# Performance work log

Measured on AMD Instinct MI355X. Metric: run time of the kernel, lower is better.

## Reference

```python
import jax, jax.numpy as jnp
import numpy as np

K = 5
BN_EPS = 1e-5


def _knn(xyz1, xyz2, embedding_lens):
    # squared pairwise distances [B, N, S]
    d2 = (jnp.sum(xyz1 ** 2, -1)[:, :, None]
          + jnp.sum(xyz2 ** 2, -1)[:, None, :]
          - 2.0 * jnp.einsum('bnc,bsc->bns', xyz1, xyz2))
    S = xyz2.shape[1]
    valid2 = jnp.arange(S)[None, :] < embedding_lens[:, None]  # [B, S]
    d2 = jnp.where(valid2[:, None, :], d2, jnp.float32(1e10))
    neg, idx = jax.lax.top_k(-d2, K)  # K smallest distances
    return -neg, idx  # squared dists [B,N,K], indices [B,N,K]


def _masked_bn(x, mask_f, gamma, beta):
    # x: [B, N, C]; mask_f: [B, N, 1] float; stats over valid positions only
    cnt = jnp.sum(mask_f)
    mean = jnp.sum(x * mask_f, axis=(0, 1)) / cnt
    var = jnp.sum(((x - mean) ** 2) * mask_f, axis=(0, 1)) / cnt
    return (x - mean) * jax.lax.rsqrt(var + BN_EPS) * gamma + beta


def setup_inputs() -> dict:
    key = jax.random.key(0)
    ks = jax.random.split(key, 8)
    B, N, S, D1, D2 = 16, 2048, 512, 384, 384
    xyz1 = jax.random.normal(ks[0], (B, N, 3), jnp.float32)
    xyz2 = jax.random.normal(ks[1], (B, S, 3), jnp.float32)
    points1 = jax.random.normal(ks[2], (B, N, D1), jnp.float32)
    points2 = jax.random.normal(ks[3], (B, S, D2), jnp.float32)
    point_lens = jax.random.randint(ks[4], (B,), N // 2, N + 1).astype(jnp.int32)
    embedding_lens = jax.random.randint(ks[5], (B,), S // 2, S + 1).astype(jnp.int32)
    point_mask = jnp.arange(N)[None, :] < point_lens[:, None]  # [B, N] bool
    Cin = D1 + D2
    W0 = jax.random.normal(ks[6], (768, Cin), jnp.float32) * (1.0 / np.sqrt(Cin))
    W1 = jax.random.normal(ks[7], (384, 768), jnp.float32) * (1.0 / np.sqrt(768))
    return dict(xyz1=xyz1, xyz2=xyz2, points1=points1, points2=points2,
                point_lens=point_lens, embedding_lens=embedding_lens,
                point_mask=point_mask,
                W0=W0, g0=jnp.ones((768,), jnp.float32), b0=jnp.zeros((768,), jnp.float32),
                W1=W1, g1=jnp.ones((384,), jnp.float32), b1=jnp.zeros((384,), jnp.float32))


def reference(xyz1, xyz2, points1, points2, point_lens, embedding_lens,
              point_mask, W0, g0, b0, W1, g1, b1):
    B, N, _ = xyz1.shape
    D2 = points2.shape[-1]
    dists, idx = _knn(xyz1[..., :3], xyz2, embedding_lens)
    eps = jnp.finfo(dists.dtype).eps
    dist_recip = 1.0 / (dists + eps)                    # [B, N, K]
    weight = dist_recip / jnp.sum(dist_recip, axis=2, keepdims=True)
    # masked gather: points2[b, idx[b,n,k], :] -> [B, N, K, D2]
    gathered = jnp.take_along_axis(points2, idx.reshape(B, N * K)[..., None],
                                   axis=1).reshape(B, N, K, D2)
    interp = jnp.sum(gathered * weight[..., None], axis=2)  # [B, N, D2]
    x = jnp.concatenate([points1, interp], axis=-1)          # [B, N, D1+D2]
    mask_f = point_mask.astype(x.dtype)[..., None]           # [B, N, 1]
    for W, g, b in ((W0, g0, b0), (W1, g1, b1)):
        x = jnp.einsum('bnc,dc->bnd', x, W)  # 1x1 conv, no bias
        x = jax.nn.relu(_masked_bn(x, mask_f, g, b))
    return x
```

## Files before the change

### kernel.cpp

```cpp
#include <hip/hip_runtime.h>
#include <cstdint>
#include <cstddef>

typedef unsigned short u16;
typedef __bf16 bf16x8 __attribute__((ext_vector_type(8)));
typedef float    f32x4 __attribute__((ext_vector_type(4)));
typedef unsigned int u32x4 __attribute__((ext_vector_type(4)));

constexpr int BB   = 16;
constexpr int NN   = 2048;
constexpr int SS   = 512;
constexpr int DD   = 384;
constexpr int CIN  = 768;
constexpr int HID  = 768;
constexpr int OUTC = 384;
constexpr int MROWS = BB * NN;
constexpr float KNN_EPS = 1.1920929e-07f;
constexpr float BN_EPS  = 1e-5f;

constexpr size_t OFF_W0B  = 0;
constexpr size_t OFF_W1B  = OFF_W0B  + (size_t)HID*CIN*2;
constexpr size_t OFF_IDX  = OFF_W1B  + (size_t)OUTC*HID*2;
constexpr size_t OFF_WGT  = OFF_IDX  + (size_t)MROWS*5*4;
constexpr size_t OFF_SUM1 = OFF_WGT  + (size_t)MROWS*5*4;
constexpr size_t OFF_SUM2 = OFF_SUM1 + (size_t)HID*2*4;
constexpr size_t OFF_COEF1= OFF_SUM2 + (size_t)OUTC*2*4;
constexpr size_t OFF_COEF2= OFF_COEF1+ (size_t)HID*2*4;
constexpr size_t OFF_XCAT = OFF_COEF2+ (size_t)OUTC*2*4;
constexpr size_t OFF_H1   = OFF_XCAT + (size_t)MROWS*CIN*2;

__device__ inline float bf2f(u16 u){ unsigned int i = ((unsigned int)u)<<16; float f; __builtin_memcpy(&f,&i,4); return f; }
__device__ inline u16 f2bf(float f){ unsigned int x; __builtin_memcpy(&x,&f,4);
  unsigned int r = (x + 0x7fffu + ((x>>16)&1u)) >> 16; return (u16)r; }

__device__ inline void async16(const void* g, void* l){
  __builtin_amdgcn_global_load_lds((const __attribute__((address_space(1))) void*)g,
                                   (__attribute__((address_space(3))) void*)l, 16, 0, 0);
}

__global__ void cvtw_kernel(const float* __restrict__ W0, const float* __restrict__ W1,
                            u16* __restrict__ W0b, u16* __restrict__ W1b){
  int t = blockIdx.x*256 + threadIdx.x;
  if (t < HID*CIN)  W0b[t] = f2bf(W0[t]);
  if (t < OUTC*HID) W1b[t] = f2bf(W1[t]);
}

__global__ __launch_bounds__(256) void knn_kernel(const float* __restrict__ xyz1,
                                                  const float* __restrict__ xyz2,
                                                  const int* __restrict__ elens,
                                                  int* __restrict__ idxO, float* __restrict__ wO){
  __shared__ f32x4 sp[SS];
  const int tid = threadIdx.x;
  const int wv = tid >> 6, lane = tid & 63;
  const int wg = blockIdx.x*4 + wv;
  const int b = wg >> 11;
  const int n = wg & (NN-1);
  for (int s = tid; s < SS; s += 256){
    float x = xyz2[((size_t)b*SS + s)*3 + 0];
    float y = xyz2[((size_t)b*SS + s)*3 + 1];
    float z = xyz2[((size_t)b*SS + s)*3 + 2];
    f32x4 v; v[0]=x; v[1]=y; v[2]=z; v[3]=x*x+y*y+z*z;
    sp[s]=v;
  }
  __syncthreads();
  const size_t qoff = ((size_t)b*NN + n)*3;
  const float qx = xyz1[qoff+0], qy = xyz1[qoff+1], qz = xyz1[qoff+2];
  const float qq = qx*qx + qy*qy + qz*qz;
  const int Sl = elens[b];

  float d0=1e30f,d1=1e30f,d2v=1e30f,d3=1e30f,d4=1e30f;
  int   i0=0,i1=0,i2=0,i3=0,i4=0;
  #pragma unroll
  for (int j=0;j<8;j++){
    const int s = lane + j*64;
    f32x4 v = sp[s];
    float d = (s < Sl) ? (qq + v[3] - 2.f*(qx*v[0] + qy*v[1] + qz*v[2])) : 1e30f;
    bool lt4=d<d4, lt3=d<d3, lt2=d<d2v, lt1=d<d1, lt0=d<d0;
    float nd4 = lt3 ? d3 : (lt4 ? d : d4); int ni4 = lt3 ? i3 : (lt4 ? s : i4);
    float nd3 = lt2 ? d2v: (lt3 ? d : d3); int ni3 = lt2 ? i2 : (lt3 ? s : i3);
    float nd2 = lt1 ? d1 : (lt2 ? d : d2v);int ni2 = lt1 ? i1 : (lt2 ? s : i2);
    float nd1 = lt0 ? d0 : (lt1 ? d : d1); int ni1 = lt0 ? i0 : (lt1 ? s : i1);
    float nd0 = lt0 ? d  : d0;             int ni0 = lt0 ? s  : i0;
    d4=nd4;i4=ni4; d3=nd3;i3=ni3; d2v=nd2;i2=ni2; d1=nd1;i1=ni1; d0=nd0;i0=ni0;
  }
  float outd[5]; int outi[5];
  #pragma unroll
  for (int r=0;r<5;r++){
    float bd = d0; int bs = i0;
    #pragma unroll
    for (int m=1;m<64;m<<=1){
      float od = __shfl_xor(bd, m, 64);
      int   os = __shfl_xor(bs, m, 64);
      if (od < bd || (od == bd && os < bs)){ bd = od; bs = os; }
    }
    outd[r]=bd; outi[r]=bs;
    if (d0 == bd && i0 == bs){ d0=d1;i0=i1; d1=d2v;i1=i2; d2v=d3;i2=i3; d3=d4;i3=i4; d4=1e30f;i4=0; }
  }
  if (lane == 0){
    float r0=1.f/(outd[0]+KNN_EPS), r1=1.f/(outd[1]+KNN_EPS), r2=1.f/(outd[2]+KNN_EPS),
          r3=1.f/(outd[3]+KNN_EPS), r4=1.f/(outd[4]+KNN_EPS);
    float inv = 1.f/(r0+r1+r2+r3+r4);
    size_t base = (size_t)wg*5;
    idxO[base+0]=outi[0]; idxO[base+1]=outi[1]; idxO[base+2]=outi[2]; idxO[base+3]=outi[3]; idxO[base+4]=outi[4];
    wO[base+0]=r0*inv; wO[base+1]=r1*inv; wO[base+2]=r2*inv; wO[base+3]=r3*inv; wO[base+4]=r4*inv;
  }
}

__global__ __launch_bounds__(384) void xcat_kernel(const float* __restrict__ p1,
                                                   const float* __restrict__ p2,
                                                   const int* __restrict__ idx,
                                                   const float* __restrict__ wgt,
                                                   u16* __restrict__ xcat){
  const int c = threadIdx.x;
  const int rowbase = blockIdx.x*8;
  for (int i=0;i<8;i++){
    const int row = rowbase + i;
    const int b = row >> 11;
    float v1 = p1[(size_t)row*DD + c];
    xcat[(size_t)row*CIN + c] = f2bf(v1);
    float acc = 0.f;
    size_t ib = (size_t)row*5;
    #pragma unroll
    for (int k=0;k<5;k++){
      int id = idx[ib+k]; float w = wgt[ib+k];
      acc += w * p2[((size_t)b*SS + id)*DD + c];
    }
    xcat[(size_t)row*CIN + DD + c] = f2bf(acc);
  }
}

__global__ __launch_bounds__(512) void gemm1_kernel(const u16* __restrict__ A,
                                                    const u16* __restrict__ Bw,
                                                    u16* __restrict__ Cout,
                                                    const int* __restrict__ plen,
                                                    float* __restrict__ sums){
  constexpr int K   = CIN;
  constexpr int NC  = HID;
  constexpr int GXX = NC/128;
  constexpr int NT  = K/32;
  constexpr int NWG = (MROWS/256)*GXX;
  constexpr int CPX = NWG/8;
  __shared__ u16 Ash[3][8192];
  __shared__ u16 Bsh[2][4096];

  const int tid  = threadIdx.x;
  const int lane = tid & 63, wv = tid >> 6;
  const int wr = wv >> 2, wc = wv & 3;
  const int l15 = lane & 15, l16 = lane >> 4;
  const int swz = (l15 >> 1) & 3;

  const int logical = (blockIdx.x & 7)*CPX + (blockIdx.x >> 3);
  const int bn = logical % GXX, bm = logical / GXX;

  const int chA0 = tid,      rA0 = chA0 >> 2, kA0 = (chA0 & 3) ^ ((chA0 >> 3) & 3);
  const int chA1 = 512+tid,  rA1 = chA1 >> 2, kA1 = (chA1 & 3) ^ ((chA1 >> 3) & 3);
  const int chB  = tid,      rB  = chB  >> 2, kB  = (chB  & 3) ^ ((chB  >> 3) & 3);
  const u16* gA0 = A  + (size_t)(bm*256 + rA0)*K + kA0*8;
  const u16* gA1 = A  + (size_t)(bm*256 + rA1)*K + kA1*8;
  const u16* gB  = Bw + (size_t)(bn*128 + rB )*K + kB*8;

  auto stageA = [&](int tt, int ab){
    async16(gA0 + tt*32, (char*)&Ash[ab][0] + wv*1024);
    async16(gA1 + tt*32, (char*)&Ash[ab][0] + 8192 + wv*1024);
  };
  auto stageB = [&](int tt, int bb){
    async16(gB + tt*32, (char*)&Bsh[bb][0] + wv*1024);
  };

  int aoff[8], boff[2];
  #pragma unroll
  for (int m=0;m<8;m++) aoff[m] = (wr*128 + m*16 + l15)*32 + ((l16 ^ swz) << 3);
  #pragma unroll
  for (int n=0;n<2;n++) boff[n] = (wc*32 + n*16 + l15)*32 + ((l16 ^ swz) << 3);

  f32x4 acc[8][2] = {};

  stageA(0, 0); stageB(0, 0); stageA(1, 1);
  asm volatile("s_waitcnt vmcnt(2)" ::: "memory");
  __builtin_amdgcn_s_barrier();

  auto step = [&](int t, int ab, int bb, int bbn, int abn2){
    if (t+1 < NT) stageB(t+1, bbn);
    if (t+2 < NT) stageA(t+2, abn2);
    bf16x8 af[8], bfr[2];
    #pragma unroll
    for (int n=0;n<2;n++) bfr[n] = *reinterpret_cast<const bf16x8*>(&Bsh[bb][boff[n]]);
    #pragma unroll
    for (int m=0;m<8;m++) af[m] = *reinterpret_cast<const bf16x8*>(&Ash[ab][aoff[m]]);
    __builtin_amdgcn_s_setprio(1);
    #pragma unroll
    for (int m=0;m<8;m++)
      #pragma unroll
      for (int n=0;n<2;n++)
        acc[m][n] = __builtin_amdgcn_mfma_f32_16x16x32_bf16(af[m], bfr[n], acc[m][n], 0, 0, 0);
    __builtin_amdgcn_s_setprio(0);
    asm volatile("s_waitcnt vmcnt(2)" ::: "memory");
    __builtin_amdgcn_s_barrier();
  };

  for (int t0=0; t0<NT; t0+=6){
    step(t0+0, 0, 0, 1, 2);
    step(t0+1, 1, 1, 0, 0);
    step(t0+2, 2, 0, 1, 1);
    step(t0+3, 0, 1, 0, 2);
    step(t0+4, 1, 0, 1, 0);
    step(t0+5, 2, 1, 0, 1);
  }

  #pragma unroll
  for (int m=0;m<8;m++){
    int r0 = bm*256 + wr*128 + m*16 + l16*4;
    #pragma unroll
    for (int n=0;n<2;n++){
      int c = bn*128 + wc*32 + n*16 + l15;
      #pragma unroll
      for (int r=0;r<4;r++)
        Cout[(size_t)(r0+r)*NC + c] = f2bf(acc[m][n][r]);
    }
  }

  const int pl = plen[bm >> 3];
  const int rbase = (bm & 7)*256 + wr*128 + l16*4;
  float cs[2] = {0.f,0.f}, cs2[2] = {0.f,0.f};
  #pragma unroll
  for (int m=0;m<8;m++){
    #pragma unroll
    for (int r=0;r<4;r++){
      if (rbase + m*16 + r < pl){
        #pragma unroll
        for (int n=0;n<2;n++){
          float v = acc[m][n][r];
          cs[n] += v; cs2[n] += v*v;
        }
      }
    }
  }
  #pragma unroll
  for (int n=0;n<2;n++){
    cs[n]  += __shfl_xor(cs[n], 16, 64);  cs[n]  += __shfl_xor(cs[n], 32, 64);
    cs2[n] += __shfl_xor(cs2[n], 16, 64); cs2[n] += __shfl_xor(cs2[n], 32, 64);
  }
  float* lsum = (float*)&Ash[0][0];
  if (tid < 256) lsum[tid] = 0.f;
  __syncthreads();
  if (l16 == 0){
    #pragma unroll
    for (int n=0;n<2;n++){
      int col = wc*32 + n*16 + l15;
      atomicAdd(&lsum[col], cs[n]);
      atomicAdd(&lsum[128 + col], cs2[n]);
    }
  }
  __syncthreads();
  if (tid < 128)       atomicAdd(&sums[bn*128 + tid], lsum[tid]);
  else if (tid < 256)  atomicAdd(&sums[NC + bn*128 + (tid-128)], lsum[tid]);
}

__global__ __launch_bounds__(256) void gemm2_kernel(const u16* __restrict__ A,
                                                    const u16* __restrict__ Bw,
                                                    float* __restrict__ Cout,
                                                    const int* __restrict__ plen,
                                                    float* __restrict__ sums,
                                                    const float* __restrict__ cf){
  constexpr int GX = 3;
  constexpr int K  = HID;
  constexpr int NC = GX*128;
  constexpr int NSTEP = K/32;
  constexpr int NWG = GX*256;
  constexpr int CPX = NWG/8;
  __shared__ u16 As[2][128*32];
  __shared__ u16 Bs[2][128*32];
  const int tid  = threadIdx.x;
  const int lane = tid & 63, wv = tid >> 6;
  const int wr = wv >> 1, wc = wv & 1;
  const int l15 = lane & 15, l16 = lane >> 4;

  const int logical = (blockIdx.x & 7)*CPX + (blockIdx.x >> 3);
  const int bn = logical % GX, bm = logical / GX;

  int rowS[2], c8S[2];
  const u16* Ab[2]; const u16* Bb[2];
  #pragma unroll
  for (int j=0;j<2;j++){
    int ch = j*256 + wv*64 + lane;
    rowS[j] = ch >> 2; c8S[j] = ch & 3;
    Ab[j] = A  + (size_t)(bm*128 + rowS[j])*K + c8S[j]*8;
    Bb[j] = Bw + (size_t)(bn*128 + rowS[j])*K + c8S[j]*8;
  }

  auto stageB = [&](int nb, int kt){
    #pragma unroll
    for (int j=0;j<2;j++)
      async16(Bb[j] + kt*32, (char*)&Bs[nb][0] + (j*256 + wv*64)*16);
  };
  u32x4 hv[2];
  auto loadA = [&](int kt){
    #pragma unroll
    for (int j=0;j<2;j++)
      hv[j] = *reinterpret_cast<const u32x4*>(Ab[j] + kt*32);
  };
  auto bnwrite = [&](int nb, int kt){
    #pragma unroll
    for (int j=0;j<2;j++){
      const int k0 = kt*32 + c8S[j]*8;
      float av[8], bv[8];
      *reinterpret_cast<f32x4*>(av)   = *reinterpret_cast<const f32x4*>(cf + k0);
      *reinterpret_cast<f32x4*>(av+4) = *reinterpret_cast<const f32x4*>(cf + k0 + 4);
      *reinterpret_cast<f32x4*>(bv)   = *reinterpret_cast<const f32x4*>(cf + K + k0);
      *reinterpret_cast<f32x4*>(bv+4) = *reinterpret_cast<const f32x4*>(cf + K + k0 + 4);
      u32x4 v = hv[j]; u32x4 o;
      #pragma unroll
      for (int q=0;q<4;q++){
        float lo = bf2f((u16)(v[q] & 0xffffu));
        float hi = bf2f((u16)(v[q] >> 16));
        lo = fmaxf(lo*av[2*q]   + bv[2*q],   0.f);
        hi = fmaxf(hi*av[2*q+1] + bv[2*q+1], 0.f);
        o[q] = (unsigned int)f2bf(lo) | ((unsigned int)f2bf(hi) << 16);
      }
      *reinterpret_cast<u32x4*>((char*)&As[nb][0] + (j*256 + wv*64)*16 + lane*16) = o;
    }
  };

  f32x4 acc[4][4] = {};

  loadA(0);
  stageB(0, 0);
  bnwrite(0, 0);
  __syncthreads();

  int cur = 0;
  for (int kt=0; kt<NSTEP; ++kt){
    const bool pf = (kt+1 < NSTEP);
    if (pf){
      loadA(kt+1);
      stageB(cur^1, kt+1);
    }
    bf16x8 af[4], bfr[4];
    #pragma unroll
    for (int m=0;m<4;m++){
      int r = wr*64 + m*16 + l15;
      af[m] = *reinterpret_cast<const bf16x8*>(&As[cur][r*32 + l16*8]);
    }
    #pragma unroll
    for (int n=0;n<4;n++){
      int c = wc*64 + n*16 + l15;
      bfr[n] = *reinterpret_cast<const bf16x8*>(&Bs[cur][c*32 + l16*8]);
    }
    #pragma unroll
    for (int m=0;m<4;m++)
      #pragma unroll
      for (int n=0;n<4;n++)
        acc[m][n] = __builtin_amdgcn_mfma_f32_16x16x32_bf16(af[m], bfr[n], acc[m][n], 0, 0, 0);
    if (pf) bnwrite(cur^1, kt+1);
    __syncthreads();
    cur ^= 1;
  }

  #pragma unroll
  for (int m=0;m<4;m++){
    int r0 = bm*128 + wr*64 + m*16 + l16*4;
    #pragma unroll
    for (int n=0;n<4;n++){
      int c = bn*128 + wc*64 + n*16 + l15;
      #pragma unroll
      for (int r=0;r<4;r++)
        Cout[(size_t)(r0+r)*NC + c] = acc[m][n][r];
    }
  }

  const int pl = plen[bm >> 4];
  const int rbase = (bm & 15)*128 + wr*64 + l16*4;
  float cs[4] = {0.f,0.f,0.f,0.f}, cs2[4] = {0.f,0.f,0.f,0.f};
  #pragma unroll
  for (int m=0;m<4;m++){
    #pragma unroll
    for (int r=0;r<4;r++){
      if (rbase + m*16 + r < pl){
        #pragma unroll
        for (int n=0;n<4;n++){
          float v = acc[m][n][r];
          cs[n] += v; cs2[n] += v*v;
        }
      }
    }
  }
  #pragma unroll
  for (int n=0;n<4;n++){
    cs[n]  += __shfl_xor(cs[n], 16, 64);  cs[n]  += __shfl_xor(cs[n], 32, 64);
    cs2[n] += __shfl_xor(cs2[n], 16, 64); cs2[n] += __shfl_xor(cs2[n], 32, 64);
  }
  float* lsum = (float*)&As[0][0];
  lsum[tid] = 0.f;
  __syncthreads();
  if (l16 == 0){
    #pragma unroll
    for (int n=0;n<4;n++){
      int col = wc*64 + n*16 + l15;
      atomicAdd(&lsum[col], cs[n]);
      atomicAdd(&lsum[128 + col], cs2[n]);
    }
  }
  __syncthreads();
  if (tid < 128)       atomicAdd(&sums[bn*128 + tid], lsum[tid]);
  else                 atomicAdd(&sums[NC + bn*128 + (tid-128)], lsum[tid]);
}

__global__ void coef_kernel(const float* __restrict__ sums, const int* __restrict__ plen,
                            const float* __restrict__ g, const float* __restrict__ bta,
                            float* __restrict__ coef, int C){
  int c = threadIdx.x;
  if (c >= C) return;
  float cnt = 0.f;
  for (int b=0;b<BB;b++) cnt += (float)plen[b];
  float mean = sums[c] / cnt;
  float var  = sums[C + c] / cnt - mean*mean;
  var = fmaxf(var, 0.f);
  float a = g[c] * rsqrtf(var + BN_EPS);
  coef[c] = a;
  coef[C + c] = bta[c] - mean*a;
}

__global__ __launch_bounds__(256) void final_kernel(float* __restrict__ Y,
                                                    const float* __restrict__ coef){
  size_t t = (size_t)blockIdx.x*256 + threadIdx.x;
  size_t f = t*4;
  int c = (int)(f % (size_t)OUTC);
  f32x4 v = *reinterpret_cast<const f32x4*>(Y + f);
  #pragma unroll
  for (int j=0;j<4;j++)
    v[j] = fmaxf(v[j]*coef[c+j] + coef[OUTC+c+j], 0.f);
  *reinterpret_cast<f32x4*>(Y + f) = v;
}

extern "C" void kernel_launch(void* const* d_in, const int* in_sizes, int n_in,
                              void* d_out, int out_size, void* d_ws, size_t ws_size,
                              hipStream_t stream){
  (void)in_sizes; (void)n_in; (void)out_size; (void)ws_size;
  const float* xyz1 = (const float*)d_in[0];
  const float* xyz2 = (const float*)d_in[1];
  const float* p1   = (const float*)d_in[2];
  const float* p2   = (const float*)d_in[3];
  const int*   plen = (const int*)d_in[4];
  const int*   elen = (const int*)d_in[5];
  const float* W0   = (const float*)d_in[7];
  const float* g0   = (const float*)d_in[8];
  const float* b0   = (const float*)d_in[9];
  const float* W1   = (const float*)d_in[10];
  const float* g1   = (const float*)d_in[11];
  const float* b1   = (const float*)d_in[12];
  float* out = (float*)d_out;
  char*  ws  = (char*)d_ws;

  u16*   W0b  = (u16*)  (ws + OFF_W0B);
  u16*   W1b  = (u16*)  (ws + OFF_W1B);
  int*   idxb = (int*)  (ws + OFF_IDX);
  float* wgtb = (float*)(ws + OFF_WGT);
  float* sum1 = (float*)(ws + OFF_SUM1);
  float* sum2 = (float*)(ws + OFF_SUM2);
  float* coef1= (float*)(ws + OFF_COEF1);
  float* coef2= (float*)(ws + OFF_COEF2);
  u16*   xcat = (u16*)  (ws + OFF_XCAT);
  u16*   h1   = (u16*)  (ws + OFF_H1);

  hipMemsetAsync(ws + OFF_SUM1, 0, (size_t)(HID*2 + OUTC*2)*4, stream);

  cvtw_kernel<<<(HID*CIN + 255)/256, 256, 0, stream>>>(W0, W1, W0b, W1b);
  knn_kernel<<<MROWS/4, 256, 0, stream>>>(xyz1, xyz2, elen, idxb, wgtb);
  xcat_kernel<<<MROWS/8, 384, 0, stream>>>(p1, p2, idxb, wgtb, xcat);

  gemm1_kernel<<<(MROWS/256)*(HID/128), 512, 0, stream>>>(xcat, W0b, h1, plen, sum1);
  coef_kernel<<<1, HID, 0, stream>>>(sum1, plen, g0, b0, coef1, HID);

  gemm2_kernel<<<3*256, 256, 0, stream>>>(h1, W1b, out, plen, sum2, coef1);
  coef_kernel<<<1, OUTC, 0, stream>>>(sum2, plen, g1, b1, coef2, OUTC);
  final_kernel<<<(size_t)MROWS*OUTC/4/256, 256, 0, stream>>>(out, coef2);
}
```

Before: 209.0 us.

## Retile gemm1 to 128x128 tiles and fuse final BN/ReLU into cooperative gemm2

gemm1 moves from 256x128 tiles with 512 threads and a triple-buffered A to 128x128 tiles with 256 threads, double buffering and a split-phase MFMA schedule, which raises workgroup count and occupancy. gemm2 becomes a cooperative kernel that keeps its accumulators in registers, does a grid-wide sync after the column-statistics atomics, then computes the BN coefficients and writes ReLU'd output directly. This removes the separate coef and final kernels and the fp32 output round trip. The cost is a grid barrier that needs all 768 blocks resident, with a fallback to the old three-kernel path if the cooperative launch fails.

```diff
diff --git a/kernel.cpp b/kernel.cpp
--- a/kernel.cpp
+++ b/kernel.cpp
@@ -1,6 +1,9 @@
 #include <hip/hip_runtime.h>
+#include <hip/hip_cooperative_groups.h>
 #include <cstdint>
 #include <cstddef>
+
+namespace cg = cooperative_groups;
 
 typedef unsigned short u16;
 typedef __bf16 bf16x8 __attribute__((ext_vector_type(8)));
@@ -129,106 +132,125 @@
   }
 }
 
-__global__ __launch_bounds__(512) void gemm1_kernel(const u16* __restrict__ A,
-                                                    const u16* __restrict__ Bw,
-                                                    u16* __restrict__ Cout,
-                                                    const int* __restrict__ plen,
-                                                    float* __restrict__ sums){
+__global__ __launch_bounds__(256, 4) void gemm1_kernel(const u16* __restrict__ A,
+                                                       const u16* __restrict__ Bw,
+                                                       u16* __restrict__ Cout,
+                                                       const int* __restrict__ plen,
+                                                       float* __restrict__ sums){
   constexpr int K   = CIN;
   constexpr int NC  = HID;
-  constexpr int GXX = NC/128;
+  constexpr int GX  = NC/128;
   constexpr int NT  = K/32;
-  constexpr int NWG = (MROWS/256)*GXX;
+  constexpr int NWG = GX*256;
   constexpr int CPX = NWG/8;
-  __shared__ u16 Ash[3][8192];
-  __shared__ u16 Bsh[2][4096];
-
+  __shared__ u16 Ash[2][128*32];
+  __shared__ u16 Bsh[2][128*32];
   const int tid  = threadIdx.x;
   const int lane = tid & 63, wv = tid >> 6;
-  const int wr = wv >> 2, wc = wv & 3;
+  const int wr = wv >> 1, wc = wv & 1;
   const int l15 = lane & 15, l16 = lane >> 4;
   const int swz = (l15 >> 1) & 3;
 
   const int logical = (blockIdx.x & 7)*CPX + (blockIdx.x >> 3);
-  const int bn = logical % GXX, bm = logical / GXX;
-
-  const int chA0 = tid,      rA0 = chA0 >> 2, kA0 = (chA0 & 3) ^ ((chA0 >> 3) & 3);
-  const int chA1 = 512+tid,  rA1 = chA1 >> 2, kA1 = (chA1 & 3) ^ ((chA1 >> 3) & 3);
-  const int chB  = tid,      rB  = chB  >> 2, kB  = (chB  & 3) ^ ((chB  >> 3) & 3);
-  const u16* gA0 = A  + (size_t)(bm*256 + rA0)*K + kA0*8;
-  const u16* gA1 = A  + (size_t)(bm*256 + rA1)*K + kA1*8;
-  const u16* gB  = Bw + (size_t)(bn*128 + rB )*K + kB*8;
-
-  auto stageA = [&](int tt, int ab){
-    async16(gA0 + tt*32, (char*)&Ash[ab][0] + wv*1024);
-    async16(gA1 + tt*32, (char*)&Ash[ab][0] + 8192 + wv*1024);
+  const int bn = logical % GX, bm = logical / GX;
+
+  const int srow = tid >> 2;
+  const int sk4  = (tid & 3) ^ ((tid >> 3) & 3);
+  const u16* gA = A  + (size_t)(bm*128 + srow)*K + sk4*8;
+  const u16* gB = Bw + (size_t)(bn*128 + srow)*K + sk4*8;
+  const int dst0 = (wv*64)*16;
+  const int dst1 = (256 + wv*64)*16;
+
+  auto stageA = [&](int tt, int bi){
+    async16(gA + tt*32,        (char*)&Ash[bi][0] + dst0);
+    async16(gA + tt*32 + 64*K, (char*)&Ash[bi][0] + dst1);
   };
-  auto stageB = [&](int tt, int bb){
-    async16(gB + tt*32, (char*)&Bsh[bb][0] + wv*1024);
+  auto stageB = [&](int tt, int bi){
+    async16(gB + tt*32,        (char*)&Bsh[bi][0] + dst0);
+    async16(gB + tt*32 + 64*K, (char*)&Bsh[bi][0] + dst1);
   };
 
-  int aoff[8], boff[2];
-  #pragma unroll
-  for (int m=0;m<8;m++) aoff[m] = (wr*128 + m*16 + l15)*32 + ((l16 ^ swz) << 3);
-  #pragma unroll
-  for (int n=0;n<2;n++) boff[n] = (wc*32 + n*16 + l15)*32 + ((l16 ^ swz) << 3);
-
-  f32x4 acc[8][2] = {};
-
-  stageA(0, 0); stageB(0, 0); stageA(1, 1);
-  asm volatile("s_waitcnt vmcnt(2)" ::: "memory");
+  int aoff[4], boff[4];
+  #pragma unroll
+  for (int m=0;m<4;m++) aoff[m] = (wr*64 + m*16 + l15)*32 + ((l16 ^ swz) << 3);
+  #pragma unroll
+  for (int n=0;n<4;n++) boff[n] = (wc*64 + n*16 + l15)*32 + ((l16 ^ swz) << 3);
+
+  f32x4 acc[4][4] = {};
+
+  stageA(0,0); stageB(0,0); stageA(1,1); stageB(1,1);
+  asm volatile("s_waitcnt vmcnt(4)" ::: "memory");
   __builtin_amdgcn_s_barrier();
-
-  auto step = [&](int t, int ab, int bb, int bbn, int abn2){
-    if (t+1 < NT) stageB(t+1, bbn);
-    if (t+2 < NT) stageA(t+2, abn2);
-    bf16x8 af[8], bfr[2];
-    #pragma unroll
-    for (int n=0;n<2;n++) bfr[n] = *reinterpret_cast<const bf16x8*>(&Bsh[bb][boff[n]]);
-    #pragma unroll
-    for (int m=0;m<8;m++) af[m] = *reinterpret_cast<const bf16x8*>(&Ash[ab][aoff[m]]);
+  __builtin_amdgcn_sched_barrier(0);
+
+  for (int t=0; t<NT; ++t){
+    const int cur = t & 1;
+    const int tt = (t+2 < NT) ? (t+2) : (NT-1);
+    bf16x8 af0 = *reinterpret_cast<const bf16x8*>(&Ash[cur][aoff[0]]);
+    bf16x8 af1 = *reinterpret_cast<const bf16x8*>(&Ash[cur][aoff[1]]);
+    bf16x8 af2 = *reinterpret_cast<const bf16x8*>(&Ash[cur][aoff[2]]);
+    bf16x8 af3 = *reinterpret_cast<const bf16x8*>(&Ash[cur][aoff[3]]);
+    bf16x8 bv0 = *reinterpret_cast<const bf16x8*>(&Bsh[cur][boff[0]]);
+    bf16x8 bv1 = *reinterpret_cast<const bf16x8*>(&Bsh[cur][boff[1]]);
+    asm volatile("s_waitcnt lgkmcnt(0)" ::: "memory");
+    __builtin_amdgcn_s_barrier();
+    __builtin_amdgcn_sched_barrier(0);
+    stageA(tt, cur);
     __builtin_amdgcn_s_setprio(1);
-    #pragma unroll
-    for (int m=0;m<8;m++)
-      #pragma unroll
-      for (int n=0;n<2;n++)
-        acc[m][n] = __builtin_amdgcn_mfma_f32_16x16x32_bf16(af[m], bfr[n], acc[m][n], 0, 0, 0);
+    acc[0][0] = __builtin_amdgcn_mfma_f32_16x16x32_bf16(af0, bv0, acc[0][0], 0,0,0);
+    acc[1][0] = __builtin_amdgcn_mfma_f32_16x16x32_bf16(af1, bv0, acc[1][0], 0,0,0);
+    acc[2][0] = __builtin_amdgcn_mfma_f32_16x16x32_bf16(af2, bv0, acc[2][0], 0,0,0);
+    acc[3][0] = __builtin_amdgcn_mfma_f32_16x16x32_bf16(af3, bv0, acc[3][0], 0,0,0);
+    acc[0][1] = __builtin_amdgcn_mfma_f32_16x16x32_bf16(af0, bv1, acc[0][1], 0,0,0);
+    acc[1][1] = __builtin_amdgcn_mfma_f32_16x16x32_bf16(af1, bv1, acc[1][1], 0,0,0);
+    acc[2][1] = __builtin_amdgcn_mfma_f32_16x16x32_bf16(af2, bv1, acc[2][1], 0,0,0);
+    acc[3][1] = __builtin_amdgcn_mfma_f32_16x16x32_bf16(af3, bv1, acc[3][1], 0,0,0);
     __builtin_amdgcn_s_setprio(0);
-    asm volatile("s_waitcnt vmcnt(2)" ::: "memory");
+    bf16x8 bv2 = *reinterpret_cast<const bf16x8*>(&Bsh[cur][boff[2]]);
+    bf16x8 bv3 = *reinterpret_cast<const bf16x8*>(&Bsh[cur][boff[3]]);
+    asm volatile("s_waitcnt lgkmcnt(0)" ::: "memory");
     __builtin_amdgcn_s_barrier();
-  };
-
-  for (int t0=0; t0<NT; t0+=6){
-    step(t0+0, 0, 0, 1, 2);
-    step(t0+1, 1, 1, 0, 0);
-    step(t0+2, 2, 0, 1, 1);
-    step(t0+3, 0, 1, 0, 2);
-    step(t0+4, 1, 0, 1, 0);
-    step(t0+5, 2, 1, 0, 1);
-  }
-
-  #pragma unroll
-  for (int m=0;m<8;m++){
-    int r0 = bm*256 + wr*128 + m*16 + l16*4;
-    #pragma unroll
-    for (int n=0;n<2;n++){
-      int c = bn*128 + wc*32 + n*16 + l15;
+    __builtin_amdgcn_sched_barrier(0);
+    stageB(tt, cur);
+    __builtin_amdgcn_s_setprio(1);
+    acc[0][2] = __builtin_amdgcn_mfma_f32_16x16x32_bf16(af0, bv2, acc[0][2], 0,0,0);
+    acc[1][2] = __builtin_amdgcn_mfma_f32_16x16x32_bf16(af1, bv2, acc[1][2], 0,0,0);
+    acc[2][2] = __builtin_amdgcn_mfma_f32_16x16x32_bf16(af2, bv2, acc[2][2], 0,0,0);
+    acc[3][2] = __builtin_amdgcn_mfma_f32_16x16x32_bf16(af3, bv2, acc[3][2], 0,0,0);
+    acc[0][3] = __builtin_amdgcn_mfma_f32_16x16x32_bf16(af0, bv3, acc[0][3], 0,0,0);
+    acc[1][3] = __builtin_amdgcn_mfma_f32_16x16x32_bf16(af1, bv3, acc[1][3], 0,0,0);
+    acc[2][3] = __builtin_amdgcn_mfma_f32_16x16x32_bf16(af2, bv3, acc[2][3], 0,0,0);
+    acc[3][3] = __builtin_amdgcn_mfma_f32_16x16x32_bf16(af3, bv3, acc[3][3], 0,0,0);
+    __builtin_amdgcn_s_setprio(0);
+    asm volatile("s_waitcnt vmcnt(4)" ::: "memory");
+    __builtin_amdgcn_s_barrier();
+    __builtin_amdgcn_sched_barrier(0);
+  }
+  asm volatile("s_waitcnt vmcnt(0)" ::: "memory");
+  __syncthreads();
+
+  #pragma unroll
+  for (int m=0;m<4;m++){
+    int r0 = bm*128 + wr*64 + m*16 + l16*4;
+    #pragma unroll
+    for (int n=0;n<4;n++){
+      int c = bn*128 + wc*64 + n*16 + l15;
       #pragma unroll
       for (int r=0;r<4;r++)
         Cout[(size_t)(r0+r)*NC + c] = f2bf(acc[m][n][r]);
     }
   }
 
-  const int pl = plen[bm >> 3];
-  const int rbase = (bm & 7)*256 + wr*128 + l16*4;
-  float cs[2] = {0.f,0.f}, cs2[2] = {0.f,0.f};
-  #pragma unroll
-  for (int m=0;m<8;m++){
+  const int pl = plen[bm >> 4];
+  const int rbase = (bm & 15)*128 + wr*64 + l16*4;
+  float cs[4] = {0.f,0.f,0.f,0.f}, cs2[4] = {0.f,0.f,0.f,0.f};
+  #pragma unroll
+  for (int m=0;m<4;m++){
     #pragma unroll
     for (int r=0;r<4;r++){
       if (rbase + m*16 + r < pl){
         #pragma unroll
-        for (int n=0;n<2;n++){
+        for (int n=0;n<4;n++){
           float v = acc[m][n][r];
           cs[n] += v; cs2[n] += v*v;
         }
@@ -236,35 +258,53 @@
     }
   }
   #pragma unroll
-  for (int n=0;n<2;n++){
+  for (int n=0;n<4;n++){
     cs[n]  += __shfl_xor(cs[n], 16, 64);  cs[n]  += __shfl_xor(cs[n], 32, 64);
     cs2[n] += __shfl_xor(cs2[n], 16, 64); cs2[n] += __shfl_xor(cs2[n], 32, 64);
   }
   float* lsum = (float*)&Ash[0][0];
-  if (tid < 256) lsum[tid] = 0.f;
+  lsum[tid] = 0.f;
   __syncthreads();
   if (l16 == 0){
     #pragma unroll
-    for (int n=0;n<2;n++){
-      int col = wc*32 + n*16 + l15;
+    for (int n=0;n<4;n++){
+      int col = wc*64 + n*16 + l15;
       atomicAdd(&lsum[col], cs[n]);
       atomicAdd(&lsum[128 + col], cs2[n]);
     }
   }
   __syncthreads();
   if (tid < 128)       atomicAdd(&sums[bn*128 + tid], lsum[tid]);
-  else if (tid < 256)  atomicAdd(&sums[NC + bn*128 + (tid-128)], lsum[tid]);
-}
-
-__global__ __launch_bounds__(256) void gemm2_kernel(const u16* __restrict__ A,
-                                                    const u16* __restrict__ Bw,
-                                                    float* __restrict__ Cout,
-                                                    const int* __restrict__ plen,
-                                                    float* __restrict__ sums,
-                                                    const float* __restrict__ cf){
+  else                 atomicAdd(&sums[NC + bn*128 + (tid-128)], lsum[tid]);
+}
+
+__global__ void coef_kernel(const float* __restrict__ sums, const int* __restrict__ plen,
+                            const float* __restrict__ g, const float* __restrict__ bta,
+                            float* __restrict__ coef, int C){
+  int c = threadIdx.x;
+  if (c >= C) return;
+  float cnt = 0.f;
+  for (int b=0;b<BB;b++) cnt += (float)plen[b];
+  float mean = sums[c] / cnt;
+  float var  = sums[C + c] / cnt - mean*mean;
+  var = fmaxf(var, 0.f);
+  float a = g[c] * rsqrtf(var + BN_EPS);
+  coef[c] = a;
+  coef[C + c] = bta[c] - mean*a;
+}
+
+template<bool COOP>
+__device__ __forceinline__ void gemm2_body(const u16* __restrict__ A,
+                                           const u16* __restrict__ Bw,
+                                           float* __restrict__ Cout,
+                                           const int* __restrict__ plen,
+                                           float* __restrict__ sums,
+                                           const float* __restrict__ cf,
+                                           const float* __restrict__ gam,
+                                           const float* __restrict__ bet){
   constexpr int GX = 3;
   constexpr int K  = HID;
-  constexpr int NC = GX*128;
+  constexpr int NC = OUTC;
   constexpr int NSTEP = K/32;
   constexpr int NWG = GX*256;
   constexpr int CPX = NWG/8;
@@ -278,14 +318,14 @@
   const int logical = (blockIdx.x & 7)*CPX + (blockIdx.x >> 3);
   const int bn = logical % GX, bm = logical / GX;
 
-  int rowS[2], c8S[2];
+  int c8S[2];
   const u16* Ab[2]; const u16* Bb[2];
   #pragma unroll
   for (int j=0;j<2;j++){
     int ch = j*256 + wv*64 + lane;
-    rowS[j] = ch >> 2; c8S[j] = ch & 3;
-    Ab[j] = A  + (size_t)(bm*128 + rowS[j])*K + c8S[j]*8;
-    Bb[j] = Bw + (size_t)(bn*128 + rowS[j])*K + c8S[j]*8;
+    int rowS = ch >> 2; c8S[j] = ch & 3;
+    Ab[j] = A  + (size_t)(bm*128 + rowS)*K + c8S[j]*8;
+    Bb[j] = Bw + (size_t)(bn*128 + rowS)*K + c8S[j]*8;
   }
 
   auto stageB = [&](int nb, int kt){
@@ -356,15 +396,17 @@
     cur ^= 1;
   }
 
-  #pragma unroll
-  for (int m=0;m<4;m++){
-    int r0 = bm*128 + wr*64 + m*16 + l16*4;
-    #pragma unroll
-    for (int n=0;n<4;n++){
-      int c = bn*128 + wc*64 + n*16 + l15;
+  if (!COOP){
+    #pragma unroll
+    for (int m=0;m<4;m++){
+      int r0 = bm*128 + wr*64 + m*16 + l16*4;
       #pragma unroll
-      for (int r=0;r<4;r++)
-        Cout[(size_t)(r0+r)*NC + c] = acc[m][n][r];
+      for (int n=0;n<4;n++){
+        int c = bn*128 + wc*64 + n*16 + l15;
+        #pragma unroll
+        for (int r=0;r<4;r++)
+          Cout[(size_t)(r0+r)*NC + c] = acc[m][n][r];
+      }
     }
   }
 
@@ -403,21 +445,55 @@
   __syncthreads();
   if (tid < 128)       atomicAdd(&sums[bn*128 + tid], lsum[tid]);
   else                 atomicAdd(&sums[NC + bn*128 + (tid-128)], lsum[tid]);
-}
-
-__global__ void coef_kernel(const float* __restrict__ sums, const int* __restrict__ plen,
-                            const float* __restrict__ g, const float* __restrict__ bta,
-                            float* __restrict__ coef, int C){
-  int c = threadIdx.x;
-  if (c >= C) return;
-  float cnt = 0.f;
-  for (int b=0;b<BB;b++) cnt += (float)plen[b];
-  float mean = sums[c] / cnt;
-  float var  = sums[C + c] / cnt - mean*mean;
-  var = fmaxf(var, 0.f);
-  float a = g[c] * rsqrtf(var + BN_EPS);
-  coef[c] = a;
-  coef[C + c] = bta[c] - mean*a;
+
+  if (COOP){
+    __threadfence();
+    cg::this_grid().sync();
+    float* s = (float*)&As[0][0];
+    if (tid < 128)      s[tid]       = atomicAdd(&sums[bn*128 + tid], 0.f);
+    else                s[tid]       = atomicAdd(&sums[NC + bn*128 + (tid-128)], 0.f);
+    __syncthreads();
+    float cnt = 0.f;
+    #pragma unroll
+    for (int b=0;b<BB;b++) cnt += (float)plen[b];
+    const float icnt = 1.f / cnt;
+    #pragma unroll
+    for (int n=0;n<4;n++){
+      const int cl = wc*64 + n*16 + l15;
+      const int col = bn*128 + cl;
+      float mean = s[cl] * icnt;
+      float var  = fmaxf(s[128+cl]*icnt - mean*mean, 0.f);
+      float a = gam[col] * rsqrtf(var + BN_EPS);
+      float c = bet[col] - mean*a;
+      #pragma unroll
+      for (int m=0;m<4;m++){
+        int r0 = bm*128 + wr*64 + m*16 + l16*4;
+        #pragma unroll
+        for (int r=0;r<4;r++)
+          Cout[(size_t)(r0+r)*NC + col] = fmaxf(acc[m][n][r]*a + c, 0.f);
+      }
+    }
+  }
+}
+
+__global__ __launch_bounds__(256, 3) void gemm2c_kernel(const u16* __restrict__ A,
+                                                        const u16* __restrict__ Bw,
+                                                        float* __restrict__ Cout,
+                                                        const int* __restrict__ plen,
+                                                        float* __restrict__ sums,
+                                                        const float* __restrict__ cf,
+                                                        const float* __restrict__ gam,
+                                                        const float* __restrict__ bet){
+  gemm2_body<true>(A, Bw, Cout, plen, sums, cf, gam, bet);
+}
+
+__global__ __launch_bounds__(256) void gemm2f_kernel(const u16* __restrict__ A,
+                                                     const u16* __restrict__ Bw,
+                                                     float* __restrict__ Cout,
+                                                     const int* __restrict__ plen,
+                                                     float* __restrict__ sums,
+                                                     const float* __restrict__ cf){
+  gemm2_body<false>(A, Bw, Cout, plen, sums, cf, nullptr, nullptr);
 }
 
 __global__ __launch_bounds__(256) void final_kernel(float* __restrict__ Y,
@@ -468,10 +544,18 @@
   knn_kernel<<<MROWS/4, 256, 0, stream>>>(xyz1, xyz2, elen, idxb, wgtb);
   xcat_kernel<<<MROWS/8, 384, 0, stream>>>(p1, p2, idxb, wgtb, xcat);
 
-  gemm1_kernel<<<(MROWS/256)*(HID/128), 512, 0, stream>>>(xcat, W0b, h1, plen, sum1);
+  gemm1_kernel<<<6*256, 256, 0, stream>>>(xcat, W0b, h1, plen, sum1);
   coef_kernel<<<1, HID, 0, stream>>>(sum1, plen, g0, b0, coef1, HID);
 
-  gemm2_kernel<<<3*256, 256, 0, stream>>>(h1, W1b, out, plen, sum2, coef1);
-  coef_kernel<<<1, OUTC, 0, stream>>>(sum2, plen, g1, b1, coef2, OUTC);
-  final_kernel<<<(size_t)MROWS*OUTC/4/256, 256, 0, stream>>>(out, coef2);
-}
+  const u16* a = h1; const u16* bw = W1b;
+  void* ka[8];
+  ka[0] = (void*)&a;    ka[1] = (void*)&bw;    ka[2] = (void*)&out;  ka[3] = (void*)&plen;
+  ka[4] = (void*)&sum2; ka[5] = (void*)&coef1; ka[6] = (void*)&g1;   ka[7] = (void*)&b1;
+  hipError_t ce = hipLaunchCooperativeKernel((void*)gemm2c_kernel, dim3(768), dim3(256),
+                                             ka, 0, stream);
+  if (ce != hipSuccess){
+    gemm2f_kernel<<<768, 256, 0, stream>>>(h1, W1b, out, plen, sum2, coef1);
+    coef_kernel<<<1, OUTC, 0, stream>>>(sum2, plen, g1, b1, coef2, OUTC);
+    final_kernel<<<(size_t)MROWS*OUTC/4/256, 256, 0, stream>>>(out, coef2);
+  }
+}
```

New measurement: 324.4 us. 55.2% more time.
